# Kernel optimization log

Measured on AMD Instinct MI355X. Metric: run time of the kernel, lower is better.

## Reference

```python
import jax, jax.numpy as jnp
import numpy as np

K = 3          # kernel_size
STRIDE = 2
PAD = K // 2


def setup_inputs() -> dict:
    key = jax.random.key(0)
    k1, k2, k3 = jax.random.split(key, 3)
    B, C, H, W = 8, 64, 256, 256
    x = jax.random.normal(k1, (B, C, H, W), dtype=jnp.float32)
    # conv_sigma: Conv2d(C, C//2, 3, bias=False), kaiming_normal-ish scale
    w_sigma = jax.random.normal(k2, (C // 2, C, 3, 3), dtype=jnp.float32) * (2.0 / (9 * C)) ** 0.5
    # fc: Linear(C//2, 1)
    w_fc = jax.random.normal(k3, (1, C // 2), dtype=jnp.float32) * 0.1
    b_fc = jnp.zeros((1,), dtype=jnp.float32)
    return {"x": x, "w_sigma": w_sigma, "w_fc": w_fc, "b_fc": b_fc}


def _gaussian_kernels(sigma):
    # sigma: [B, 1] -> normalized Gaussian kernels [B, 1, K, K]
    r = jnp.arange(-PAD, PAD + 1, dtype=jnp.float32)
    d = jnp.sqrt(r[:, None] ** 2 + r[None, :] ** 2)          # [K, K] radial distance
    s = jnp.clip(sigma, 1e-4)[:, :, None, None]              # [B, 1, 1, 1]
    g = (1.0 / (jnp.sqrt(2.0 * jnp.pi) * s)) * jnp.exp(-0.5 * (d / s) ** 2)
    return g / jnp.sum(g, axis=(2, 3), keepdims=True)


def reference(x, w_sigma, w_fc, b_fc):
    B = x.shape[0]
    # sigma branch: 3x3 VALID conv -> relu -> global avgpool -> fc -> sigmoid
    h = jax.lax.conv_general_dilated(
        x, w_sigma, (1, 1), 'VALID',
        dimension_numbers=('NCHW', 'OIHW', 'NCHW'))           # [B, C/2, H-2, W-2]
    h = jax.nn.relu(h).mean(axis=(2, 3))                      # [B, C/2]
    sigma = jax.nn.sigmoid(h @ w_fc.T + b_fc)                 # [B, 1]
    kern = _gaussian_kernels(sigma)                           # [B, 1, K, K]
    # per-sample blur: treat C as batch, B as channels, grouped conv groups=B
    xp = jnp.pad(x.transpose(1, 0, 2, 3),
                 ((0, 0), (0, 0), (PAD, PAD), (PAD, PAD)), mode='reflect')
    out = jax.lax.conv_general_dilated(
        xp, kern, (STRIDE, STRIDE), 'VALID',
        dimension_numbers=('NCHW', 'OIHW', 'NCHW'),
        feature_group_count=B)                                # [C, B, H', W']
    return out
```

## Files before the change

### kernel.cpp

```cpp
#include <hip/hip_runtime.h>
#include <math.h>


typedef __attribute__((ext_vector_type(8))) short s8v;
typedef __attribute__((ext_vector_type(4))) float f4v;

static __device__ inline unsigned short f2bf(float f) {
    union { float f; unsigned int u; } v; v.f = f;
    unsigned int u = v.u;
    unsigned int r = u + 0x7FFFu + ((u >> 16) & 1u);
    return (unsigned short)(r >> 16);
}

static __device__ inline unsigned int pk_bf16(float a, float b) {
    unsigned int r;
    asm("v_cvt_pk_bf16_f32 %0, %1, %2" : "=v"(r) : "v"(a), "v"(b));
    return r;
}

__global__ void prep_kernel(const float* __restrict__ w, float* __restrict__ ws) {
    int i = blockIdx.x * blockDim.x + threadIdx.x;
    if (i < 256) ws[i] = 0.f;
    if (i < 9 * 32 * 64) {
        int ic  = i & 63;
        int oc  = (i >> 6) & 31;
        int tap = i >> 11;
        unsigned short* wtb = (unsigned short*)(ws + 512);
        wtb[i] = f2bf(w[oc * 576 + ic * 9 + tap]);
    }
}

__global__ __launch_bounds__(256, 3) void conv_mfma_kernel(
        const float* __restrict__ x, const unsigned short* __restrict__ wtb,
        float* __restrict__ acc_out) {
    __shared__ __align__(16) unsigned char sx[370 * 128];
    __shared__ float sred[4][32];

    const int bx = blockIdx.x, by = blockIdx.y, b = blockIdx.z;
    const int ox0 = bx * 32, oy0 = by * 8;
    const int tid = threadIdx.x;
    const int lane = tid & 63, w = tid >> 6;
    const int m = lane & 15, q = lane >> 4;

    const float* xb = x + (size_t)b * 64 * 65536;
    for (int i = tid; i < 1440; i += 256) {
        int ch = i % 9;
        int t9 = i / 9;
        int yy = t9 % 10;
        int r4 = t9 / 10;
        int y  = oy0 + yy;
        int xc = ox0 + ch * 4;
        if (y < 256 && xc < 256) {
            const float* src = xb + (size_t)(r4 << 2) * 65536 + y * 256 + xc;
            float4 v0 = *(const float4*)(src);
            float4 v1 = *(const float4*)(src + 65536);
            float4 v2 = *(const float4*)(src + 131072);
            float4 v3 = *(const float4*)(src + 196608);
            const float* a0 = (const float*)&v0;
            const float* a1 = (const float*)&v1;
            const float* a2 = (const float*)&v2;
            const float* a3 = (const float*)&v3;
            int p0 = yy * 37 + ch * 4;
#pragma unroll
            for (int j = 0; j < 4; ++j) {
                int p = p0 + j;
                unsigned int lo = pk_bf16(a0[j], a1[j]);
                unsigned int hi = pk_bf16(a2[j], a3[j]);
                int cw = (r4 >> 1) ^ (p & 7);
                *(uint2*)(sx + p * 128 + cw * 16 + (r4 & 1) * 8) = make_uint2(lo, hi);
            }
        }
    }
    __syncthreads();

    f4v acc[4][2];
#pragma unroll
    for (int mt = 0; mt < 4; ++mt)
#pragma unroll
        for (int nt = 0; nt < 2; ++nt) acc[mt][nt] = (f4v)0.f;

    int pb[4];
#pragma unroll
    for (int mt = 0; mt < 4; ++mt)
        pb[mt] = (2 * w + (mt >> 1)) * 37 + (mt & 1) * 16 + m;

    const unsigned short* wB = wtb + m * 64 + q * 8;

#pragma unroll
    for (int t = 0; t < 9; ++t) {
        const int off = (t / 3) * 37 + (t % 3);
        s8v b00 = *(const s8v*)(wB + t * 2048);
        s8v b01 = *(const s8v*)(wB + t * 2048 + 1024);
        s8v b10 = *(const s8v*)(wB + t * 2048 + 32);
        s8v b11 = *(const s8v*)(wB + t * 2048 + 1024 + 32);
#pragma unroll
        for (int kc = 0; kc < 2; ++kc) {
            s8v bb0 = kc ? b10 : b00;
            s8v bb1 = kc ? b11 : b01;
#pragma unroll
            for (int mt = 0; mt < 4; ++mt) {
                int p = pb[mt] + off;
                int quad = (kc * 4 + q) ^ (p & 7);
                s8v afr = *(const s8v*)(sx + p * 128 + quad * 16);
                acc[mt][0] = __builtin_amdgcn_mfma_f32_16x16x32_bf16(afr, bb0, acc[mt][0], 0, 0, 0);
                acc[mt][1] = __builtin_amdgcn_mfma_f32_16x16x32_bf16(afr, bb1, acc[mt][1], 0, 0, 0);
            }
        }
    }

    float s0 = 0.f, s1 = 0.f;
#pragma unroll
    for (int mt = 0; mt < 4; ++mt) {
        int oy = oy0 + 2 * w + (mt >> 1);
        int oxb = ox0 + (mt & 1) * 16 + q * 4;
#pragma unroll
        for (int reg = 0; reg < 4; ++reg) {
            bool val = (oxb + reg < 254) && (oy < 254);
            if (val) {
                s0 += fmaxf(acc[mt][0][reg], 0.f);
                s1 += fmaxf(acc[mt][1][reg], 0.f);
            }
        }
    }
    s0 += __shfl_xor(s0, 16, 64); s0 += __shfl_xor(s0, 32, 64);
    s1 += __shfl_xor(s1, 16, 64); s1 += __shfl_xor(s1, 32, 64);
    if (lane < 16) { sred[w][lane] = s0; sred[w][16 + lane] = s1; }
    __syncthreads();
    if (tid < 32)
        atomicAdd(&acc_out[b * 32 + tid],
                  sred[0][tid] + sred[1][tid] + sred[2][tid] + sred[3][tid]);
}

__global__ void sigma_kernel(const float* __restrict__ acc, const float* __restrict__ wfc,
                             const float* __restrict__ bfc, float* __restrict__ kout) {
    int t = threadIdx.x;
    int b = t >> 3, j = t & 7;
    float s = 0.f;
#pragma unroll
    for (int i = 0; i < 4; ++i) s += acc[b * 32 + j + i * 8] * wfc[j + i * 8];
    s += __shfl_xor(s, 4, 8);
    s += __shfl_xor(s, 2, 8);
    s += __shfl_xor(s, 1, 8);
    if (j == 0) {
        float z = s * (1.0f / (254.0f * 254.0f)) + bfc[0];
        float sig = 1.0f / (1.0f + __expf(-z));
        float ss = fmaxf(sig, 1e-4f);
        float inv2 = 0.5f / (ss * ss);
        float e1 = __expf(-inv2);
        float e2 = __expf(-2.0f * inv2);
        float inv_norm = 1.0f / (1.0f + 4.0f * e1 + 4.0f * e2);
        kout[b * 4 + 0] = inv_norm;
        kout[b * 4 + 1] = e1 * inv_norm;
        kout[b * 4 + 2] = e2 * inv_norm;
    }
}

__global__ __launch_bounds__(256) void blur_kernel(
        const float* __restrict__ x, const float* __restrict__ kp,
        float* __restrict__ out) {
    const int c = blockIdx.z, b = blockIdx.y;
    const int tid = threadIdx.x;
    const int qx = tid & 31;
    const int oy = blockIdx.x * 8 + (tid >> 5);

    const float kC = kp[b * 4 + 0];
    const float kE = kp[b * 4 + 1];
    const float kD = kp[b * 4 + 2];

    const float* xb = x + ((size_t)(b * 64 + c)) * 65536;

    float o0 = 0.f, o1 = 0.f, o2 = 0.f, o3 = 0.f;
#pragma unroll
    for (int dy = 0; dy < 3; ++dy) {
        int iy = 2 * oy + dy - 1;
        if (iy < 0) iy = 1;
        const float* row = xb + iy * 256;
        const float4 f0 = *(const float4*)(row + 8 * qx);
        const float4 f1 = *(const float4*)(row + 8 * qx + 4);
        float lf = __shfl_up(f1.w, 1, 64);
        const float sm1 = (qx == 0) ? f0.y : lf;
        const float ka = (dy == 1) ? kE : kD;
        const float kb = (dy == 1) ? kC : kE;
        const float kc2 = (dy == 1) ? kE : kD;
        o0 = fmaf(ka, sm1,  fmaf(kb, f0.x, fmaf(kc2, f0.y, o0)));
        o1 = fmaf(ka, f0.y, fmaf(kb, f0.z, fmaf(kc2, f0.w, o1)));
        o2 = fmaf(ka, f0.w, fmaf(kb, f1.x, fmaf(kc2, f1.y, o2)));
        o3 = fmaf(ka, f1.y, fmaf(kb, f1.z, fmaf(kc2, f1.w, o3)));
    }
    *(float4*)(out + (((size_t)c * 8 + b) * 128 + oy) * 128 + 4 * qx) =
        make_float4(o0, o1, o2, o3);
}

extern "C" void kernel_launch(void* const* d_in, const int* in_sizes, int n_in,
                              void* d_out, int out_size, void* d_ws, size_t ws_size,
                              hipStream_t stream) {
    const float* x       = (const float*)d_in[0];
    const float* w_sigma = (const float*)d_in[1];
    const float* w_fc    = (const float*)d_in[2];
    const float* b_fc    = (const float*)d_in[3];
    float* out = (float*)d_out;
    float* ws  = (float*)d_ws;
    const unsigned short* wtb = (const unsigned short*)(ws + 512);

    prep_kernel<<<72, 256, 0, stream>>>(w_sigma, ws);
    conv_mfma_kernel<<<dim3(8, 32, 8), 256, 0, stream>>>(x, wtb, ws);
    sigma_kernel<<<1, 64, 0, stream>>>(ws, w_fc, b_fc, ws + 256);
    blur_kernel<<<dim3(16, 8, 64), 256, 0, stream>>>(x, ws + 256, out);
}
```

Before: 267.7 us.

## Batch global loads into registers, prefetch weights, and change LDS swizzle

The conv kernel's staging loop now issues all six rounds of global float4 loads up front into registers, with clamped addresses instead of branches, and only then converts them and writes them to LDS. This raises memory-level parallelism. The per-tap weight fragments are double-buffered so the next tap's loads overlap the current MFMAs. The LDS XOR swizzle now keys on (p>>1)&7 instead of p&7, aimed at reducing bank conflicts. In exchange, register pressure rises by about 96 floats for the staged values, which could hurt occupancy under the 3-blocks launch bound.

```diff
diff --git a/kernel.cpp b/kernel.cpp
--- a/kernel.cpp
+++ b/kernel.cpp
@@ -43,30 +43,49 @@
     const int m = lane & 15, q = lane >> 4;
 
     const float* xb = x + (size_t)b * 64 * 65536;
-    for (int i = tid; i < 1440; i += 256) {
+    float4 va[6][4];
+    int   pj[6];
+    int   r4a[6];
+    bool  vld[6];
+#pragma unroll
+    for (int k = 0; k < 6; ++k) {
+        int i  = tid + k * 256;
         int ch = i % 9;
         int t9 = i / 9;
         int yy = t9 % 10;
         int r4 = t9 / 10;
-        int y  = oy0 + yy;
-        int xc = ox0 + ch * 4;
-        if (y < 256 && xc < 256) {
-            const float* src = xb + (size_t)(r4 << 2) * 65536 + y * 256 + xc;
-            float4 v0 = *(const float4*)(src);
-            float4 v1 = *(const float4*)(src + 65536);
-            float4 v2 = *(const float4*)(src + 131072);
-            float4 v3 = *(const float4*)(src + 196608);
-            const float* a0 = (const float*)&v0;
-            const float* a1 = (const float*)&v1;
-            const float* a2 = (const float*)&v2;
-            const float* a3 = (const float*)&v3;
-            int p0 = yy * 37 + ch * 4;
+        int y  = oy0 + yy;  if (y > 255) y = 255;
+        int xc = ox0 + ch * 4;  if (xc > 252) xc = 252;
+        const float* src = xb + (size_t)((r4 & 15) << 2) * 65536 + y * 256 + xc;
+        va[k][0] = *(const float4*)(src);
+        va[k][1] = *(const float4*)(src + 65536);
+        va[k][2] = *(const float4*)(src + 131072);
+        va[k][3] = *(const float4*)(src + 196608);
+        pj[k]  = yy * 37 + ch * 4;
+        r4a[k] = r4;
+        vld[k] = (i < 1440);
+    }
+
+    const unsigned short* wB = wtb + m * 64 + q * 8;
+    s8v bc0 = *(const s8v*)(wB);
+    s8v bc1 = *(const s8v*)(wB + 1024);
+    s8v bc2 = *(const s8v*)(wB + 32);
+    s8v bc3 = *(const s8v*)(wB + 1024 + 32);
+
+#pragma unroll
+    for (int k = 0; k < 6; ++k) {
+        if (vld[k]) {
+            int r4 = r4a[k];
+            const float* a0 = (const float*)&va[k][0];
+            const float* a1 = (const float*)&va[k][1];
+            const float* a2 = (const float*)&va[k][2];
+            const float* a3 = (const float*)&va[k][3];
 #pragma unroll
             for (int j = 0; j < 4; ++j) {
-                int p = p0 + j;
+                int p = pj[k] + j;
                 unsigned int lo = pk_bf16(a0[j], a1[j]);
                 unsigned int hi = pk_bf16(a2[j], a3[j]);
-                int cw = (r4 >> 1) ^ (p & 7);
+                int cw = (r4 >> 1) ^ ((p >> 1) & 7);
                 *(uint2*)(sx + p * 128 + cw * 16 + (r4 & 1) * 8) = make_uint2(lo, hi);
             }
         }
@@ -84,28 +103,34 @@
     for (int mt = 0; mt < 4; ++mt)
         pb[mt] = (2 * w + (mt >> 1)) * 37 + (mt & 1) * 16 + m;
 
-    const unsigned short* wB = wtb + m * 64 + q * 8;
-
 #pragma unroll
     for (int t = 0; t < 9; ++t) {
         const int off = (t / 3) * 37 + (t % 3);
-        s8v b00 = *(const s8v*)(wB + t * 2048);
-        s8v b01 = *(const s8v*)(wB + t * 2048 + 1024);
-        s8v b10 = *(const s8v*)(wB + t * 2048 + 32);
-        s8v b11 = *(const s8v*)(wB + t * 2048 + 1024 + 32);
-#pragma unroll
-        for (int kc = 0; kc < 2; ++kc) {
-            s8v bb0 = kc ? b10 : b00;
-            s8v bb1 = kc ? b11 : b01;
-#pragma unroll
-            for (int mt = 0; mt < 4; ++mt) {
-                int p = pb[mt] + off;
-                int quad = (kc * 4 + q) ^ (p & 7);
-                s8v afr = *(const s8v*)(sx + p * 128 + quad * 16);
-                acc[mt][0] = __builtin_amdgcn_mfma_f32_16x16x32_bf16(afr, bb0, acc[mt][0], 0, 0, 0);
-                acc[mt][1] = __builtin_amdgcn_mfma_f32_16x16x32_bf16(afr, bb1, acc[mt][1], 0, 0, 0);
-            }
-        }
+        s8v bn0, bn1, bn2, bn3;
+        if (t < 8) {
+            const unsigned short* wN = wB + (t + 1) * 2048;
+            bn0 = *(const s8v*)(wN);
+            bn1 = *(const s8v*)(wN + 1024);
+            bn2 = *(const s8v*)(wN + 32);
+            bn3 = *(const s8v*)(wN + 1024 + 32);
+        }
+#pragma unroll
+        for (int mt = 0; mt < 4; ++mt) {
+            int p  = pb[mt] + off;
+            int q0 = q ^ ((p >> 1) & 7);
+            s8v afr = *(const s8v*)(sx + p * 128 + q0 * 16);
+            acc[mt][0] = __builtin_amdgcn_mfma_f32_16x16x32_bf16(afr, bc0, acc[mt][0], 0, 0, 0);
+            acc[mt][1] = __builtin_amdgcn_mfma_f32_16x16x32_bf16(afr, bc1, acc[mt][1], 0, 0, 0);
+        }
+#pragma unroll
+        for (int mt = 0; mt < 4; ++mt) {
+            int p  = pb[mt] + off;
+            int q1 = (4 + q) ^ ((p >> 1) & 7);
+            s8v afr = *(const s8v*)(sx + p * 128 + q1 * 16);
+            acc[mt][0] = __builtin_amdgcn_mfma_f32_16x16x32_bf16(afr, bc2, acc[mt][0], 0, 0, 0);
+            acc[mt][1] = __builtin_amdgcn_mfma_f32_16x16x32_bf16(afr, bc3, acc[mt][1], 0, 0, 0);
+        }
+        if (t < 8) { bc0 = bn0; bc1 = bn1; bc2 = bn2; bc3 = bn3; }
     }
 
     float s0 = 0.f, s1 = 0.f;
```

After: 255.6 us. -4.5%, faster.

## Retile sigma conv to full-width row pairs with split input-channel halves

Applied to the files above, without the earlier changes.

The conv kernel now gives each block two output rows across the full 256-pixel width. It stages 4 input rows by 32 channels at a time in a 64KB swizzled LDS buffer, in two input-channel passes. Weights are re-laid out per channel half with next-tap prefetch, and each wave computes 8 M-tiles. This cuts the halo re-reads of the old 32x8 tiles (10x37 of 32x8) and the per-block overhead, but raises LDS use, which lowers occupancy to 2 blocks per CU, and adds a barrier between the channel halves.

```diff
diff --git a/kernel.cpp b/kernel.cpp
--- a/kernel.cpp
+++ b/kernel.cpp
@@ -21,37 +21,51 @@
 __global__ void prep_kernel(const float* __restrict__ w, float* __restrict__ ws) {
     int i = blockIdx.x * blockDim.x + threadIdx.x;
     if (i < 256) ws[i] = 0.f;
-    if (i < 9 * 32 * 64) {
-        int ic  = i & 63;
-        int oc  = (i >> 6) & 31;
-        int tap = i >> 11;
+    if (i < 18432) {
+        int icg = i / 9216;
+        int rem = i - icg * 9216;
+        int tap = rem >> 10;
+        int oc  = (rem >> 5) & 31;
+        int icl = rem & 31;
         unsigned short* wtb = (unsigned short*)(ws + 512);
-        wtb[i] = f2bf(w[oc * 576 + ic * 9 + tap]);
-    }
-}
-
-__global__ __launch_bounds__(256, 3) void conv_mfma_kernel(
+        wtb[i] = f2bf(w[oc * 576 + (icg * 32 + icl) * 9 + tap]);
+    }
+}
+
+__global__ __launch_bounds__(256, 2) void conv_mfma_kernel(
         const float* __restrict__ x, const unsigned short* __restrict__ wtb,
         float* __restrict__ acc_out) {
-    __shared__ __align__(16) unsigned char sx[370 * 128];
-    __shared__ float sred[4][32];
-
-    const int bx = blockIdx.x, by = blockIdx.y, b = blockIdx.z;
-    const int ox0 = bx * 32, oy0 = by * 8;
+    __shared__ __align__(16) unsigned char sx[65536];
+    float* sred = (float*)sx;
+
+    const int yp = blockIdx.x, b = blockIdx.y;
+    const int iy0 = 2 * yp;
     const int tid = threadIdx.x;
     const int lane = tid & 63, w = tid >> 6;
     const int m = lane & 15, q = lane >> 4;
-
     const float* xb = x + (size_t)b * 64 * 65536;
-    for (int i = tid; i < 1440; i += 256) {
-        int ch = i % 9;
-        int t9 = i / 9;
-        int yy = t9 % 10;
-        int r4 = t9 / 10;
-        int y  = oy0 + yy;
-        int xc = ox0 + ch * 4;
-        if (y < 256 && xc < 256) {
-            const float* src = xb + (size_t)(r4 << 2) * 65536 + y * 256 + xc;
+
+    const int orow = w >> 1;
+    const int pxb  = (w & 1) * 128;
+
+    f4v acc[8][2];
+#pragma unroll
+    for (int i = 0; i < 8; ++i) {
+        acc[i][0] = (f4v)0.f;
+        acc[i][1] = (f4v)0.f;
+    }
+
+#pragma unroll
+    for (int icg = 0; icg < 2; ++icg) {
+        if (icg) __syncthreads();
+
+#pragma unroll
+        for (int k = 0; k < 8; ++k) {
+            int t  = 4 * k + w;
+            int r  = t >> 3;
+            int jq = t & 7;
+            const float* src = xb + (size_t)(icg * 32 + 4 * jq) * 65536
+                                  + (iy0 + r) * 256 + 4 * lane;
             float4 v0 = *(const float4*)(src);
             float4 v1 = *(const float4*)(src + 65536);
             float4 v2 = *(const float4*)(src + 131072);
@@ -60,75 +74,64 @@
             const float* a1 = (const float*)&v1;
             const float* a2 = (const float*)&v2;
             const float* a3 = (const float*)&v3;
-            int p0 = yy * 37 + ch * 4;
-#pragma unroll
-            for (int j = 0; j < 4; ++j) {
-                int p = p0 + j;
-                unsigned int lo = pk_bf16(a0[j], a1[j]);
-                unsigned int hi = pk_bf16(a2[j], a3[j]);
-                int cw = (r4 >> 1) ^ (p & 7);
-                *(uint2*)(sx + p * 128 + cw * 16 + (r4 & 1) * 8) = make_uint2(lo, hi);
+#pragma unroll
+            for (int u = 0; u < 4; ++u) {
+                int pxrow = r * 256 + 4 * lane + u;
+                int C = pxrow * 4 + (jq >> 1);
+                C ^= (C >> 4) & 7;
+                *(uint2*)(sx + C * 16 + (jq & 1) * 8) =
+                    make_uint2(pk_bf16(a0[u], a1[u]), pk_bf16(a2[u], a3[u]));
             }
         }
-    }
-    __syncthreads();
-
-    f4v acc[4][2];
-#pragma unroll
-    for (int mt = 0; mt < 4; ++mt)
-#pragma unroll
-        for (int nt = 0; nt < 2; ++nt) acc[mt][nt] = (f4v)0.f;
-
-    int pb[4];
-#pragma unroll
-    for (int mt = 0; mt < 4; ++mt)
-        pb[mt] = (2 * w + (mt >> 1)) * 37 + (mt & 1) * 16 + m;
-
-    const unsigned short* wB = wtb + m * 64 + q * 8;
-
-#pragma unroll
-    for (int t = 0; t < 9; ++t) {
-        const int off = (t / 3) * 37 + (t % 3);
-        s8v b00 = *(const s8v*)(wB + t * 2048);
-        s8v b01 = *(const s8v*)(wB + t * 2048 + 1024);
-        s8v b10 = *(const s8v*)(wB + t * 2048 + 32);
-        s8v b11 = *(const s8v*)(wB + t * 2048 + 1024 + 32);
-#pragma unroll
-        for (int kc = 0; kc < 2; ++kc) {
-            s8v bb0 = kc ? b10 : b00;
-            s8v bb1 = kc ? b11 : b01;
-#pragma unroll
-            for (int mt = 0; mt < 4; ++mt) {
-                int p = pb[mt] + off;
-                int quad = (kc * 4 + q) ^ (p & 7);
-                s8v afr = *(const s8v*)(sx + p * 128 + quad * 16);
-                acc[mt][0] = __builtin_amdgcn_mfma_f32_16x16x32_bf16(afr, bb0, acc[mt][0], 0, 0, 0);
-                acc[mt][1] = __builtin_amdgcn_mfma_f32_16x16x32_bf16(afr, bb1, acc[mt][1], 0, 0, 0);
-            }
+
+        const unsigned short* wg = wtb + icg * 9216;
+        s8v b0 = *(const s8v*)(wg + m * 32 + q * 8);
+        s8v b1 = *(const s8v*)(wg + (16 + m) * 32 + q * 8);
+        __syncthreads();
+
+#pragma unroll
+        for (int tp = 0; tp < 9; ++tp) {
+            const int dy = tp / 3, dx = tp % 3;
+            s8v bn0, bn1;
+            if (tp < 8) {
+                const unsigned short* wn = wg + (tp + 1) * 1024;
+                bn0 = *(const s8v*)(wn + m * 32 + q * 8);
+                bn1 = *(const s8v*)(wn + (16 + m) * 32 + q * 8);
+            }
+#pragma unroll
+            for (int i = 0; i < 8; ++i) {
+                int prw = (orow + dy) * 256 + pxb + i * 16 + m + dx;
+                if (prw > 1023) prw = 1023;
+                int C = prw * 4 + q;
+                C ^= (C >> 4) & 7;
+                s8v afr = *(const s8v*)(sx + C * 16);
+                acc[i][0] = __builtin_amdgcn_mfma_f32_16x16x32_bf16(afr, b0, acc[i][0], 0, 0, 0);
+                acc[i][1] = __builtin_amdgcn_mfma_f32_16x16x32_bf16(afr, b1, acc[i][1], 0, 0, 0);
+            }
+            if (tp < 8) { b0 = bn0; b1 = bn1; }
         }
     }
 
     float s0 = 0.f, s1 = 0.f;
 #pragma unroll
-    for (int mt = 0; mt < 4; ++mt) {
-        int oy = oy0 + 2 * w + (mt >> 1);
-        int oxb = ox0 + (mt & 1) * 16 + q * 4;
+    for (int i = 0; i < 8; ++i) {
 #pragma unroll
         for (int reg = 0; reg < 4; ++reg) {
-            bool val = (oxb + reg < 254) && (oy < 254);
-            if (val) {
-                s0 += fmaxf(acc[mt][0][reg], 0.f);
-                s1 += fmaxf(acc[mt][1][reg], 0.f);
+            int px = pxb + i * 16 + q * 4 + reg;
+            if (px < 254) {
+                s0 += fmaxf(acc[i][0][reg], 0.f);
+                s1 += fmaxf(acc[i][1][reg], 0.f);
             }
         }
     }
     s0 += __shfl_xor(s0, 16, 64); s0 += __shfl_xor(s0, 32, 64);
     s1 += __shfl_xor(s1, 16, 64); s1 += __shfl_xor(s1, 32, 64);
-    if (lane < 16) { sred[w][lane] = s0; sred[w][16 + lane] = s1; }
+    __syncthreads();
+    if (lane < 16) { sred[w * 32 + lane] = s0; sred[w * 32 + 16 + lane] = s1; }
     __syncthreads();
     if (tid < 32)
         atomicAdd(&acc_out[b * 32 + tid],
-                  sred[0][tid] + sred[1][tid] + sred[2][tid] + sred[3][tid]);
+                  sred[tid] + sred[32 + tid] + sred[64 + tid] + sred[96 + tid]);
 }
 
 __global__ void sigma_kernel(const float* __restrict__ acc, const float* __restrict__ wfc,
@@ -203,7 +206,7 @@
     const unsigned short* wtb = (const unsigned short*)(ws + 512);
 
     prep_kernel<<<72, 256, 0, stream>>>(w_sigma, ws);
-    conv_mfma_kernel<<<dim3(8, 32, 8), 256, 0, stream>>>(x, wtb, ws);
+    conv_mfma_kernel<<<dim3(127, 8), 256, 0, stream>>>(x, wtb, ws);
     sigma_kernel<<<1, 64, 0, stream>>>(ws, w_fc, b_fc, ws + 256);
     blur_kernel<<<dim3(16, 8, 64), 256, 0, stream>>>(x, ws + 256, out);
 }
```

Measured after the change: 242.6 us. 1.1x faster.
